# Optimization experiments

Measured on AMD Instinct MI355X. Metric: run time of the kernel, lower is better.

## Reference

```python
import jax, jax.numpy as jnp
import numpy as np

B, L, D = 8, 4096, 768


def setup_inputs() -> dict:
    key = jax.random.key(0)
    k1, = jax.random.split(key, 1)
    x = jax.random.normal(k1, (B, L, D), dtype=jnp.float32)
    alpha = jnp.ones((L, 1), dtype=jnp.float32)  # nn.Parameter(torch.ones(l_dim, 1))
    return {"x": x, "alpha": alpha}


def reference(x, alpha):
    # Original: y = (x @ x^T).mean(-1, keepdim=True) / D
    # Algebraically identical (mean over j of sum_d x_i,d x_j,d = x_i . mean_j x_j):
    d = x.shape[-1]
    l = x.shape[1]
    mean_x = jnp.mean(x, axis=1)                       # [B, D]
    y = jnp.einsum('bld,bd->bl', x, mean_x)[..., None] / d  # [B, L, 1]
    # Original: y = (y @ y^T).mean(-1, keepdim=True) / L
    # (y y^T)_ij = y_i * y_j; mean over j = y_i * mean(y)
    y = y * jnp.mean(y, axis=1, keepdims=True) / l     # [B, L, 1]
    # y * x + alpha  (alpha broadcast over batch and D); dropout p=0 -> identity
    return alpha + y * x
```

## Files before the change

kernel.cpp:

```cpp
#include <hip/hip_runtime.h>

constexpr int Bn = 8;
constexpr int Ln = 4096;
constexpr int Dn = 768;
constexpr int D4 = Dn / 4;
constexpr int CPB = 128;
constexpr int CHUNKS_TOT = Bn * CPB;
constexpr int RPC = Ln / CPB;

typedef float vfloat4 __attribute__((ext_vector_type(4)));

__global__ __launch_bounds__(192)
void k_colsum_part(const float4* __restrict__ x, float4* __restrict__ part) {
    const int ch = blockIdx.x;
    const int t  = threadIdx.x;
    const float4* p = x + (size_t)ch * RPC * D4 + t;
    float4 s = {0.f, 0.f, 0.f, 0.f};
    #pragma unroll 8
    for (int l = 0; l < RPC; ++l) {
        float4 v = p[(size_t)l * D4];
        s.x += v.x; s.y += v.y; s.z += v.z; s.w += v.w;
    }
    part[(size_t)ch * D4 + t] = s;
}

__global__ __launch_bounds__(64)
void k_colsum_fold(const float* __restrict__ part, float* __restrict__ colsum) {
    const int b    = blockIdx.x / 12;
    const int sl   = blockIdx.x % 12;
    const int lane = threadIdx.x;
    const float* pb = part + (size_t)b * CPB * Dn + sl * 64 + lane;
    float s = 0.f;
    #pragma unroll 8
    for (int c = 0; c < CPB; ++c) s += pb[(size_t)c * Dn];
    colsum[b * Dn + sl * 64 + lane] = s;
}

__global__ __launch_bounds__(256)
void k_fused(const float4* __restrict__ x, const float4* __restrict__ colsum,
             const float* __restrict__ alpha, vfloat4* __restrict__ out) {
    const int wave = threadIdx.x >> 6;
    const int lane = threadIdx.x & 63;
    const int row  = blockIdx.x * 4 + wave;
    const int b    = row >> 12;
    const int l    = row & (Ln - 1);

    const float4* cs = colsum + (size_t)b * D4;
    float4 c0 = cs[lane], c1 = cs[lane + 64], c2 = cs[lane + 128];

    float ssq = c0.x * c0.x + c0.y * c0.y + c0.z * c0.z + c0.w * c0.w
              + c1.x * c1.x + c1.y * c1.y + c1.z * c1.z + c1.w * c1.w
              + c2.x * c2.x + c2.y * c2.y + c2.z * c2.z + c2.w * c2.w;
    #pragma unroll
    for (int off = 1; off < 64; off <<= 1) ssq += __shfl_xor(ssq, off);

    const float4* xr = x + (size_t)row * D4;
    float4 x0 = xr[lane], x1 = xr[lane + 64], x2 = xr[lane + 128];

    float acc = x0.x * c0.x + x0.y * c0.y + x0.z * c0.z + x0.w * c0.w
              + x1.x * c1.x + x1.y * c1.y + x1.z * c1.z + x1.w * c1.w
              + x2.x * c2.x + x2.y * c2.y + x2.z * c2.z + x2.w * c2.w;
    #pragma unroll
    for (int off = 1; off < 64; off <<= 1) acc += __shfl_xor(acc, off);

    const float f1 = 1.0f / ((float)Ln * (float)Dn);
    const float k  = ssq * f1 * f1 / ((float)Ln * (float)Ln);
    const float coef = acc * k;

    const float a = alpha[l];
    vfloat4* orow = out + (size_t)row * D4;
    vfloat4 o0 = {a + coef * x0.x, a + coef * x0.y, a + coef * x0.z, a + coef * x0.w};
    vfloat4 o1 = {a + coef * x1.x, a + coef * x1.y, a + coef * x1.z, a + coef * x1.w};
    vfloat4 o2 = {a + coef * x2.x, a + coef * x2.y, a + coef * x2.z, a + coef * x2.w};
    __builtin_nontemporal_store(o0, &orow[lane]);
    __builtin_nontemporal_store(o1, &orow[lane + 64]);
    __builtin_nontemporal_store(o2, &orow[lane + 128]);
}

extern "C" void kernel_launch(void* const* d_in, const int* in_sizes, int n_in,
                              void* d_out, int out_size, void* d_ws, size_t ws_size,
                              hipStream_t stream) {
    const float* x     = (const float*)d_in[0];
    const float* alpha = (const float*)d_in[1];
    float* out = (float*)d_out;

    float* part   = (float*)d_ws;
    float* colsum = part + (size_t)CHUNKS_TOT * Dn;

    k_colsum_part<<<CHUNKS_TOT, 192, 0, stream>>>((const float4*)x, (float4*)part);
    k_colsum_fold<<<Bn * 12, 64, 0, stream>>>(part, colsum);
    k_fused<<<(Bn * Ln) / 4, 256, 0, stream>>>((const float4*)x, (const float4*)colsum,
                                               alpha, (vfloat4*)out);
}
```

Before: 196.4 us.

## Fuse column-sum and output pass into one cooperative kernel with grid sync

Replaces the three-kernel pipeline with a single cooperative kernel. Each block sums its slice of rows into per-batch column sums via atomics, synchronizes the grid, then re-reads the same rows to compute and write the output. The intent is to cut launch overhead and get cache reuse of x between the two phases. The cost is a grid-wide barrier, atomic contention, an extra memset, and reliance on all 2048 blocks being co-resident, with the old path kept as a fallback.

```diff
diff --git a/kernel.cpp b/kernel.cpp
--- a/kernel.cpp
+++ b/kernel.cpp
@@ -1,14 +1,82 @@
 #include <hip/hip_runtime.h>
+#include <hip/hip_cooperative_groups.h>
+
+namespace cg = cooperative_groups;
 
 constexpr int Bn = 8;
 constexpr int Ln = 4096;
 constexpr int Dn = 768;
 constexpr int D4 = Dn / 4;
+
+typedef float vfloat4 __attribute__((ext_vector_type(4)));
+
+constexpr int TPB    = 192;
+constexpr int BLOCKS = 2048;
+constexpr int BPB    = BLOCKS / Bn;
+constexpr int RPB    = Ln / BPB;
+
+__global__ __launch_bounds__(TPB, 3)
+void k_all(const float4* __restrict__ x, const float* __restrict__ alpha,
+           vfloat4* __restrict__ out, float* __restrict__ colsum) {
+    cg::grid_group grid = cg::this_grid();
+    const int t    = threadIdx.x;
+    const int b    = blockIdx.x / BPB;
+    const int sub  = blockIdx.x % BPB;
+    const int row0 = b * Ln + sub * RPB;
+
+    const float4* p = x + (size_t)row0 * D4 + t;
+    float4 s = {0.f, 0.f, 0.f, 0.f};
+    #pragma unroll 8
+    for (int l = 0; l < RPB; ++l) {
+        float4 v = p[(size_t)l * D4];
+        s.x += v.x; s.y += v.y; s.z += v.z; s.w += v.w;
+    }
+    float* cb = colsum + b * Dn + t * 4;
+    atomicAdd(cb + 0, s.x);
+    atomicAdd(cb + 1, s.y);
+    atomicAdd(cb + 2, s.z);
+    atomicAdd(cb + 3, s.w);
+
+    grid.sync();
+
+    const float4* cs = (const float4*)(colsum + b * Dn);
+    float4 cm = cs[t];
+    float ssq = cm.x * cm.x + cm.y * cm.y + cm.z * cm.z + cm.w * cm.w;
+    #pragma unroll
+    for (int off = 1; off < 64; off <<= 1) ssq += __shfl_xor(ssq, off);
+    __shared__ float wsum[3];
+    const int wave = t >> 6, lane = t & 63;
+    if (lane == 0) wsum[wave] = ssq;
+    __syncthreads();
+    const float f1 = 1.0f / ((float)Ln * (float)Dn);
+    const float scale = (wsum[0] + wsum[1] + wsum[2]) * f1 * f1
+                        / ((float)Ln * (float)Ln);
+
+    float4 c0 = cs[lane], c1 = cs[lane + 64], c2 = cs[lane + 128];
+    for (int r = wave; r < RPB; r += 3) {
+        const int row = row0 + r;
+        const float4* xr = x + (size_t)row * D4;
+        float4 x0 = xr[lane], x1 = xr[lane + 64], x2 = xr[lane + 128];
+        float acc = x0.x * c0.x + x0.y * c0.y + x0.z * c0.z + x0.w * c0.w
+                  + x1.x * c1.x + x1.y * c1.y + x1.z * c1.z + x1.w * c1.w
+                  + x2.x * c2.x + x2.y * c2.y + x2.z * c2.z + x2.w * c2.w;
+        #pragma unroll
+        for (int off = 1; off < 64; off <<= 1) acc += __shfl_xor(acc, off);
+        const float coef = acc * scale;
+        const float a = alpha[row & (Ln - 1)];
+        vfloat4* orow = (vfloat4*)out + (size_t)row * D4;
+        vfloat4 o0 = {a + coef * x0.x, a + coef * x0.y, a + coef * x0.z, a + coef * x0.w};
+        vfloat4 o1 = {a + coef * x1.x, a + coef * x1.y, a + coef * x1.z, a + coef * x1.w};
+        vfloat4 o2 = {a + coef * x2.x, a + coef * x2.y, a + coef * x2.z, a + coef * x2.w};
+        __builtin_nontemporal_store(o0, &orow[lane]);
+        __builtin_nontemporal_store(o1, &orow[lane + 64]);
+        __builtin_nontemporal_store(o2, &orow[lane + 128]);
+    }
+}
+
 constexpr int CPB = 128;
 constexpr int CHUNKS_TOT = Bn * CPB;
 constexpr int RPC = Ln / CPB;
-
-typedef float vfloat4 __attribute__((ext_vector_type(4)));
 
 __global__ __launch_bounds__(192)
 void k_colsum_part(const float4* __restrict__ x, float4* __restrict__ part) {
@@ -47,7 +115,6 @@
 
     const float4* cs = colsum + (size_t)b * D4;
     float4 c0 = cs[lane], c1 = cs[lane + 64], c2 = cs[lane + 128];
-
     float ssq = c0.x * c0.x + c0.y * c0.y + c0.z * c0.z + c0.w * c0.w
               + c1.x * c1.x + c1.y * c1.y + c1.z * c1.z + c1.w * c1.w
               + c2.x * c2.x + c2.y * c2.y + c2.z * c2.z + c2.w * c2.w;
@@ -56,7 +123,6 @@
 
     const float4* xr = x + (size_t)row * D4;
     float4 x0 = xr[lane], x1 = xr[lane + 64], x2 = xr[lane + 128];
-
     float acc = x0.x * c0.x + x0.y * c0.y + x0.z * c0.z + x0.w * c0.w
               + x1.x * c1.x + x1.y * c1.y + x1.z * c1.z + x1.w * c1.w
               + x2.x * c2.x + x2.y * c2.y + x2.z * c2.z + x2.w * c2.w;
@@ -84,11 +150,22 @@
     const float* alpha = (const float*)d_in[1];
     float* out = (float*)d_out;
 
-    float* part   = (float*)d_ws;
-    float* colsum = part + (size_t)CHUNKS_TOT * Dn;
+    float* colsum = (float*)d_ws;
+    float* part   = colsum + (size_t)Bn * Dn;
 
-    k_colsum_part<<<CHUNKS_TOT, 192, 0, stream>>>((const float4*)x, (float4*)part);
-    k_colsum_fold<<<Bn * 12, 64, 0, stream>>>(part, colsum);
-    k_fused<<<(Bn * Ln) / 4, 256, 0, stream>>>((const float4*)x, (const float4*)colsum,
-                                               alpha, (vfloat4*)out);
+    hipMemsetAsync(colsum, 0, (size_t)Bn * Dn * sizeof(float), stream);
+
+    const float4* x4 = (const float4*)x;
+    vfloat4* out4 = (vfloat4*)out;
+    void* args[] = {(void*)&x4, (void*)&alpha, (void*)&out4, (void*)&colsum};
+    hipError_t err = hipLaunchCooperativeKernel(
+        reinterpret_cast<const void*>(k_all), dim3(BLOCKS), dim3(TPB),
+        args, 0u, stream);
+
+    if (err != hipSuccess) {
+        k_colsum_part<<<CHUNKS_TOT, 192, 0, stream>>>(x4, (float4*)part);
+        k_colsum_fold<<<Bn * 12, 64, 0, stream>>>(part, colsum);
+        k_fused<<<(Bn * Ln) / 4, 256, 0, stream>>>(x4, (const float4*)colsum,
+                                                   alpha, out4);
+    }
 }
```

Result: slower. 433.8 us (+120.9%).
